# Kernel tuning notes

Measured on AMD Instinct MI355X. Metric: run time of the kernel, lower is better.

Reference implementation:

```python
import jax, jax.numpy as jnp
import numpy as np

WORD_VOCAB = 100000
TAG_VOCAB = 50
WD = 300
TD = 100
EMB = WD + TD          # 400: LSTM input size AND hidden size
H = EMB
L = 512


def setup_inputs() -> dict:
    key = jax.random.key(0)
    ks = jax.random.split(key, 16)
    def p(k, shape):
        return jax.random.normal(k, shape, dtype=jnp.float32) * 0.05
    return {
        "words_idx_tensor": jax.random.randint(ks[0], (1, L), 0, WORD_VOCAB),
        "tags_idx_tensor": jax.random.randint(ks[1], (1, L), 0, TAG_VOCAB),
        "max_length": L,
        "word_emb": p(ks[2], (WORD_VOCAB, WD)),
        "tag_emb": p(ks[3], (TAG_VOCAB, TD)),
        # stacked [fwd, bwd] directions per layer (PyTorch LSTM gate order i,f,g,o)
        "w_ih_l0": p(ks[4], (2, 4 * H, EMB)),
        "w_hh_l0": p(ks[5], (2, 4 * H, H)),
        "b_ih_l0": p(ks[6], (2, 4 * H)),
        "b_hh_l0": p(ks[7], (2, 4 * H)),
        "w_ih_l1": p(ks[8], (2, 4 * H, 2 * H)),
        "w_hh_l1": p(ks[9], (2, 4 * H, H)),
        "b_ih_l1": p(ks[10], (2, 4 * H)),
        "b_hh_l1": p(ks[11], (2, 4 * H)),
        "fc1_w": p(ks[12], (1, 4 * H)),
        "fc1_b": p(ks[13], (1,)),
    }


def _lstm_dir(x, w_ih, w_hh, b_ih, b_hh, reverse):
    # x: [T, in]. Precompute input projections once (hoisted out of scan).
    xi = x @ w_ih.T + b_ih + b_hh  # [T, 4H]
    Hn = w_hh.shape[1]

    def step(carry, g_in):
        h, c = carry
        g = g_in + h @ w_hh.T
        i, f, gg, o = jnp.split(g, 4, axis=-1)
        c = jax.nn.sigmoid(f) * c + jax.nn.sigmoid(i) * jnp.tanh(gg)
        h = jax.nn.sigmoid(o) * jnp.tanh(c)
        return (h, c), h

    init = (jnp.zeros((Hn,), x.dtype), jnp.zeros((Hn,), x.dtype))
    _, hs = jax.lax.scan(step, init, xi, reverse=reverse)
    return hs  # [T, H]


def _bilstm(x, w_ih, w_hh, b_ih, b_hh):
    fwd = _lstm_dir(x, w_ih[0], w_hh[0], b_ih[0], b_hh[0], False)
    bwd = _lstm_dir(x, w_ih[1], w_hh[1], b_ih[1], b_hh[1], True)
    return jnp.concatenate([fwd, bwd], axis=-1)  # [T, 2H]


def reference(words_idx_tensor, tags_idx_tensor, max_length, word_emb, tag_emb,
              w_ih_l0, w_hh_l0, b_ih_l0, b_hh_l0,
              w_ih_l1, w_hh_l1, b_ih_l1, b_hh_l1,
              fc1_w, fc1_b):
    # Embedding lookup + concat; batch dim of size 1 squeezed (torch's
    # view(shape[1], shape[0], -1) yields [L, 1, emb] for the LSTM).
    x = jnp.concatenate([word_emb[words_idx_tensor[0]],
                         tag_emb[tags_idx_tensor[0]]], axis=-1)  # [L, EMB]

    h = _bilstm(x, w_ih_l0, w_hh_l0, b_ih_l0, b_hh_l0)   # [L, 2H]
    h = _bilstm(h, w_ih_l1, w_hh_l1, b_ih_l1, b_hh_l1)   # [L, 2H]

    # Pairwise edge scores: tanh(W @ [h_i; h_j] + b).
    # Split W into head/dep halves -> two small GEMMs + broadcast outer-sum,
    # avoiding the O(L^2 * 4H) concatenated feature tensor.
    two_h = fc1_w.shape[1] // 2
    s = h @ fc1_w[:, :two_h].T   # [L, 1]
    t = h @ fc1_w[:, two_h:].T   # [L, 1]
    scores = jnp.tanh(s[:, None, :] + t[None, :, :] + fc1_b)  # [L, L, 1]
    # torch stacks (i outer, j inner) -> [L*L, 1, 1]
    return scores.reshape(max_length * max_length, 1, 1)
```

## Files before the change

kernel.cpp:

```cpp
#include <hip/hip_runtime.h>

#define SEQ 512
#define HID 400
#define GATES 1600
#define E1 800
#define TEAM 25
#define RECGRID 256
#define ROWS 64
#define HSL 16

__device__ __forceinline__ float bf2f(unsigned short u) {
    return __uint_as_float(((unsigned)u) << 16);
}
__device__ __forceinline__ unsigned short f2bf(float f) {
    unsigned u = __float_as_uint(f);
    u += 0x7FFFu + ((u >> 16) & 1u);
    return (unsigned short)(u >> 16);
}
__device__ __forceinline__ float sigm(float x) { return 1.f / (1.f + __expf(-x)); }
__device__ __forceinline__ float tanh_f(float x) {
    float xc = fminf(fmaxf(x, -15.f), 15.f);
    float e = __expf(2.f * xc);
    return (e - 1.f) / (e + 1.f);
}
__device__ __forceinline__ float loadx(const void* p, size_t i, int isbf) {
    return isbf ? bf2f(((const unsigned short*)p)[i]) : ((const float*)p)[i];
}

__global__ void detect_kernel(const unsigned short* __restrict__ wemb,
                              unsigned* __restrict__ dtf) {
    __shared__ int cnt;
    if (threadIdx.x == 0) cnt = 0;
    __syncthreads();
    int pass = 0;
    for (int i = 0; i < 8; ++i) {
        unsigned short u = wemb[threadIdx.x * 8 + i];
        int e = (u >> 7) & 0xFF;
        pass += (e >= 100 && e <= 130) ? 1 : 0;
    }
    atomicAdd(&cnt, pass);
    __syncthreads();
    if (threadIdx.x == 0) *dtf = (cnt >= 1843) ? 1u : 0u;
}

__global__ void embed_kernel(const int* __restrict__ words, const int* __restrict__ tags,
                             const void* __restrict__ wemb, const void* __restrict__ temb,
                             float* __restrict__ x ,
                             const unsigned* __restrict__ dtf) {
    int t = blockIdx.x;
    int w = words[t], g = tags[t];
    int isbf = (int)*dtf;
    for (int k = threadIdx.x; k < HID; k += blockDim.x) {
        float v = (k < 300) ? loadx(wemb, (size_t)w * 300 + k, isbf)
                            : loadx(temb, (size_t)g * 100 + (k - 300), isbf);
        x[(size_t)t * HID + k] = v;
    }
}

__global__ __launch_bounds__(256) void proj_kernel(
        const void* __restrict__ Araw, int tagged,
        const void* __restrict__ Wraw ,
        const void* __restrict__ bihRaw, const void* __restrict__ bhhRaw,
        float* __restrict__ xi ,
        int K, const unsigned* __restrict__ dtf) {
    const int isbf = (int)*dtf;
    __shared__ float As[16][132];
    __shared__ float Ws[16][68];
    int tid = threadIdx.x;
    int t0 = blockIdx.x * 128, n0 = blockIdx.y * 64, dir = blockIdx.z;
    int arow = tid >> 1, akoff = (tid & 1) * 8;
    int wrow = tid >> 2, wkoff = (tid & 3) * 4;
    int tx = (tid & 15) * 4;
    int ty = (tid >> 4) * 8;

    const float* Af = (const float*)Araw + (size_t)(t0 + arow) * K + akoff;
    const unsigned long long* At = (const unsigned long long*)Araw +
                                   (size_t)(t0 + arow) * K + akoff;
    size_t wbase = (size_t)(dir * GATES + n0 + wrow) * K + wkoff;
    const float* Wf = (const float*)Wraw + wbase;
    const unsigned short* Wh = (const unsigned short*)Wraw + wbase;

    float acc[8][4] = {};
    for (int k0 = 0; k0 < K; k0 += 16) {
        float av8[8];
        if (tagged) {
            ulonglong2 q0 = *(const ulonglong2*)(At + k0);
            ulonglong2 q1 = *(const ulonglong2*)(At + k0 + 2);
            ulonglong2 q2 = *(const ulonglong2*)(At + k0 + 4);
            ulonglong2 q3 = *(const ulonglong2*)(At + k0 + 6);
            av8[0] = __uint_as_float((unsigned)q0.x); av8[1] = __uint_as_float((unsigned)q0.y);
            av8[2] = __uint_as_float((unsigned)q1.x); av8[3] = __uint_as_float((unsigned)q1.y);
            av8[4] = __uint_as_float((unsigned)q2.x); av8[5] = __uint_as_float((unsigned)q2.y);
            av8[6] = __uint_as_float((unsigned)q3.x); av8[7] = __uint_as_float((unsigned)q3.y);
        } else {
            float4 a0 = *(const float4*)(Af + k0);
            float4 a1 = *(const float4*)(Af + k0 + 4);
            av8[0] = a0.x; av8[1] = a0.y; av8[2] = a0.z; av8[3] = a0.w;
            av8[4] = a1.x; av8[5] = a1.y; av8[6] = a1.z; av8[7] = a1.w;
        }
        float4 wv;
        if (isbf) {
            ushort4 w4 = *(const ushort4*)(Wh + k0);
            wv = make_float4(bf2f(w4.x), bf2f(w4.y), bf2f(w4.z), bf2f(w4.w));
        } else {
            wv = *(const float4*)(Wf + k0);
        }
        __syncthreads();
#pragma unroll
        for (int i = 0; i < 8; ++i) As[akoff + i][arow] = av8[i];
        Ws[wkoff + 0][wrow] = wv.x; Ws[wkoff + 1][wrow] = wv.y;
        Ws[wkoff + 2][wrow] = wv.z; Ws[wkoff + 3][wrow] = wv.w;
        __syncthreads();
#pragma unroll
        for (int kk = 0; kk < 16; ++kk) {
            float4 alo = *(const float4*)&As[kk][ty];
            float4 ahi = *(const float4*)&As[kk][ty + 4];
            float4 w4  = *(const float4*)&Ws[kk][tx];
            float av[8] = {alo.x, alo.y, alo.z, alo.w, ahi.x, ahi.y, ahi.z, ahi.w};
            float wvv[4] = {w4.x, w4.y, w4.z, w4.w};
#pragma unroll
            for (int i = 0; i < 8; ++i)
#pragma unroll
                for (int j = 0; j < 4; ++j)
                    acc[i][j] = fmaf(av[i], wvv[j], acc[i][j]);
        }
    }
    float bias[4];
#pragma unroll
    for (int j = 0; j < 4; ++j) {
        int n = n0 + tx + j;
        bias[j] = loadx(bihRaw, dir * GATES + n, isbf) + loadx(bhhRaw, dir * GATES + n, isbf);
    }
    float* xout = xi + (size_t)dir * SEQ * GATES;
#pragma unroll
    for (int i = 0; i < 8; ++i) {
        int t = t0 + ty + i;
        float4 o = make_float4(acc[i][0] + bias[0], acc[i][1] + bias[1],
                               acc[i][2] + bias[2], acc[i][3] + bias[3]);
        *(float4*)&xout[(size_t)t * GATES + n0 + tx] = o;
    }
}

struct SyncArea { unsigned cnt[8]; unsigned claim[2]; unsigned pad[6]; };

__global__ __launch_bounds__(512, 2) void rec_kernel(
        const float* __restrict__ xi ,
        const void* __restrict__ whhRaw ,
        unsigned long long* __restrict__ hx  ,
        unsigned long long* __restrict__ hx2 ,
        unsigned tagbase, SyncArea* __restrict__ sy,
        const unsigned* __restrict__ dtf) {
    int tid = threadIdx.x;
    __shared__ int role[2];
    if (tid == 0) {
        unsigned xcd = __builtin_amdgcn_s_getreg((3 << 11) | 20) & 0xFu;
        unsigned rank = atomicAdd(&sy->cnt[xcd], 1u);
        unsigned group = rank / TEAM;
        unsigned key = 1u + xcd * 64u + group;
        if ((rank % TEAM) == TEAM - 1) {
            unsigned prev = atomicCAS(&sy->claim[0], 0u, key);
            if (prev != 0u) atomicCAS(&sy->claim[1], 0u, key);
        }
        int dir = -1;
        while (dir < 0) {
            unsigned c0 = __hip_atomic_load(&sy->claim[0], __ATOMIC_RELAXED,
                                            __HIP_MEMORY_SCOPE_AGENT);
            unsigned c1 = __hip_atomic_load(&sy->claim[1], __ATOMIC_RELAXED,
                                            __HIP_MEMORY_SCOPE_AGENT);
            if (c0 == key) dir = 0;
            else if (c1 == key) dir = 1;
            else if (c0 != 0u && c1 != 0u) dir = 2;
        }
        role[0] = dir;
        role[1] = (int)(rank % TEAM);
    }
    __syncthreads();
    const int dir = role[0];
    const int wg  = role[1];
    if (dir == 2) return;

    const int chunk = tid & 15;
    const int rg    = tid >> 4;
    const int isbf  = (int)*dtf;
    const int dirHID = dir * HID;

    __shared__ __align__(16) float hbuf[16 * 28];
    __shared__ __align__(16) float partials[ROWS][20];
    __shared__ __align__(16) float gates[ROWS];

    float wv[2][25];
#pragma unroll
    for (int r = 0; r < 2; ++r) {
        int lr = rg * 2 + r;
        int jj = lr >> 2, gg = lr & 3;
        int grow = gg * HID + wg * HSL + jj;
        size_t base = ((size_t)dir * GATES + grow) * HID + chunk * 25;
        if (isbf) {
            const unsigned short* p = (const unsigned short*)whhRaw + base;
#pragma unroll
            for (int c = 0; c < 25; ++c) wv[r][c] = bf2f(p[c]);
        } else {
            const float* p = (const float*)whhRaw + base;
#pragma unroll
            for (int c = 0; c < 25; ++c) wv[r][c] = p[c];
        }
    }

    int xrow = 0;
    if (tid < ROWS) { int jj = tid >> 2, gg = tid & 3; xrow = gg * HID + wg * HSL + jj; }
    const int hIdx = (tid / 25) * 28 + (tid % 25);
    const float* xibase = xi + (size_t)dir * SEQ * GATES;
    float cstate = 0.f;
    size_t myelem = dirHID + wg * HSL + tid;

#pragma unroll 1
    for (int k = 0; k < SEQ; ++k) {
        int t = dir ? (SEQ - 1 - k) : k;
        float xiv = 0.f;
        if (tid < ROWS) xiv = xibase[(size_t)t * GATES + xrow];

        if (k > 0) {
            int tprev = dir ? (t + 1) : (t - 1);
            if (tid < HID) {
                const unsigned want = tagbase + (unsigned)k;
                size_t eidx = (size_t)tprev * E1 + dirHID + tid;
                const volatile unsigned long long* p =
                    (const volatile unsigned long long*)&hx[eidx];
                unsigned long long w;
                int spin = 0;
                for (;;) {
                    w = *p;
                    if ((unsigned)(w >> 32) == want) break;
                    if (++spin >= 24) {
                        w = __hip_atomic_load(&hx2[eidx], __ATOMIC_RELAXED,
                                              __HIP_MEMORY_SCOPE_AGENT);
                        if ((unsigned)(w >> 32) == want) break;
                        spin = 0;
                    }
                }
                hbuf[hIdx] = __uint_as_float((unsigned)w);
            }
        } else {
            if (tid < HID) hbuf[hIdx] = 0.f;
        }
        __syncthreads();

        const float* hb = &hbuf[chunk * 28];
        float4 h4a = *(const float4*)(hb + 0);
        float4 h4b = *(const float4*)(hb + 4);
        float4 h4c = *(const float4*)(hb + 8);
        float4 h4d = *(const float4*)(hb + 12);
        float4 h4e = *(const float4*)(hb + 16);
        float4 h4f = *(const float4*)(hb + 20);
        float hv[25] = {h4a.x, h4a.y, h4a.z, h4a.w, h4b.x, h4b.y, h4b.z, h4b.w,
                        h4c.x, h4c.y, h4c.z, h4c.w, h4d.x, h4d.y, h4d.z, h4d.w,
                        h4e.x, h4e.y, h4e.z, h4e.w, h4f.x, h4f.y, h4f.z, h4f.w,
                        hb[24]};
        float acc0 = 0.f, acc1 = 0.f;
#pragma unroll
        for (int c = 0; c < 25; ++c) {
            acc0 = fmaf(wv[0][c], hv[c], acc0);
            acc1 = fmaf(wv[1][c], hv[c], acc1);
        }
        partials[rg * 2 + 0][chunk] = acc0;
        partials[rg * 2 + 1][chunk] = acc1;
        __syncthreads();

        if (tid < ROWS) {
            const float4* pr = (const float4*)&partials[tid][0];
            float4 p0 = pr[0], p1 = pr[1], p2 = pr[2], p3 = pr[3];
            float s = p0.x + p0.y + p0.z + p0.w
                    + p1.x + p1.y + p1.z + p1.w
                    + p2.x + p2.y + p2.z + p2.w
                    + p3.x + p3.y + p3.z + p3.w;
            gates[tid] = s + xiv;
        }
        __syncthreads();

        if (tid < HSL) {
            float4 g4 = *(const float4*)&gates[tid * 4];
            float ig = sigm(g4.x), fg = sigm(g4.y), cg = tanh_f(g4.z), og = sigm(g4.w);
            cstate = fg * cstate + ig * cg;
            float hv2 = og * tanh_f(cstate);
            unsigned long long w =
                ((unsigned long long)(tagbase + (unsigned)k + 1u) << 32) |
                (unsigned long long)(unsigned)__float_as_uint(hv2);
            size_t eidx = (size_t)t * E1 + myelem;
            *(volatile unsigned long long*)&hx[eidx] = w;
            __hip_atomic_store(&hx2[eidx], w, __ATOMIC_RELAXED,
                               __HIP_MEMORY_SCOPE_AGENT);
        }
    }
}

__global__ void st_kernel(const unsigned long long* __restrict__ h1x ,
                          const void* __restrict__ fw ,
                          float* __restrict__ sv, float* __restrict__ tv,
                          const unsigned* __restrict__ dtf) {
    int i = blockIdx.x;
    int lane = threadIdx.x;
    int isbf = (int)*dtf;
    float s = 0.f, t = 0.f;
    for (int j = lane; j < E1; j += 64) {
        float hv = __uint_as_float((unsigned)h1x[(size_t)i * E1 + j]);
        s += hv * loadx(fw, j, isbf);
        t += hv * loadx(fw, E1 + j, isbf);
    }
#pragma unroll
    for (int o = 32; o > 0; o >>= 1) {
        s += __shfl_xor(s, o, 64);
        t += __shfl_xor(t, o, 64);
    }
    if (lane == 0) { sv[i] = s; tv[i] = t; }
}

__global__ void scores_kernel(const float* __restrict__ sv, const float* __restrict__ tv,
                              const void* __restrict__ fb, void* __restrict__ out,
                              const unsigned* __restrict__ dtf) {
    int idx = blockIdx.x * blockDim.x + threadIdx.x;
    int i = idx >> 9, j = idx & 511;
    int isbf = (int)*dtf;
    float v = tanh_f(sv[i] + tv[j] + loadx(fb, 0, isbf));
    if (isbf) ((unsigned short*)out)[idx] = f2bf(v);
    else      ((float*)out)[idx] = v;
}

static constexpr size_t OFF_X    = 0;
static constexpr size_t OFF_XI   = 819200;
static constexpr size_t OFF_SV   = 7372800;
static constexpr size_t OFF_TV   = 7374848;
static constexpr size_t OFF_DTF  = 7376896;
static constexpr size_t OFF_SYNC = 7376960;
static constexpr size_t OFF_HX   = 7377216;
static constexpr size_t OFF_HX2  = 10654016;

extern "C" void kernel_launch(void* const* d_in, const int* in_sizes, int n_in,
                              void* d_out, int out_size, void* d_ws, size_t ws_size,
                              hipStream_t stream) {
    const int* words = (const int*)d_in[0];
    const int* tags  = (const int*)d_in[1];
    const void* wemb = d_in[3];
    const void* temb = d_in[4];
    const void* wih0 = d_in[5];
    const void* whh0 = d_in[6];
    const void* bih0 = d_in[7];
    const void* bhh0 = d_in[8];
    const void* wih1 = d_in[9];
    const void* whh1 = d_in[10];
    const void* bih1 = d_in[11];
    const void* bhh1 = d_in[12];
    const void* fw   = d_in[13];
    const void* fb   = d_in[14];

    char* ws = (char*)d_ws;
    float* x               = (float*)(ws + OFF_X);
    float* xi              = (float*)(ws + OFF_XI);
    float* sv              = (float*)(ws + OFF_SV);
    float* tv              = (float*)(ws + OFF_TV);
    unsigned* dtf          = (unsigned*)(ws + OFF_DTF);
    SyncArea* sync0        = (SyncArea*)(ws + OFF_SYNC);
    SyncArea* sync1        = (SyncArea*)(ws + OFF_SYNC + 64);
    unsigned long long* hx  = (unsigned long long*)(ws + OFF_HX);
    unsigned long long* hx2 = (unsigned long long*)(ws + OFF_HX2);

    hipMemsetAsync(ws + OFF_SYNC, 0, 128, stream);
    detect_kernel<<<1, 256, 0, stream>>>((const unsigned short*)wemb, dtf);
    embed_kernel<<<SEQ, 128, 0, stream>>>(words, tags, wemb, temb, x, dtf);

    proj_kernel<<<dim3(4, 25, 2), 256, 0, stream>>>(x, 0, wih0, bih0, bhh0, xi, HID, dtf);
    rec_kernel<<<RECGRID, 512, 0, stream>>>(xi, whh0, hx, hx2, 0u, sync0, dtf);

    proj_kernel<<<dim3(4, 25, 2), 256, 0, stream>>>(hx, 1, wih1, bih1, bhh1, xi, E1, dtf);
    rec_kernel<<<RECGRID, 512, 0, stream>>>(xi, whh1, hx, hx2, 512u, sync1, dtf);

    st_kernel<<<SEQ, 64, 0, stream>>>(hx, fw, sv, tv, dtf);
    scores_kernel<<<(SEQ * SEQ) / 256, 256, 0, stream>>>(sv, tv, fb, d_out, dtf);
}
```

Before: 1.791 ms.

## Use sc0 inline-asm polling, prefetch next input gates, move publishing to idle wave

Replaces the volatile loads and stores used for inter-block h exchange with inline-asm global loads and stores carrying the sc0 cache bit, and raises the spin count before falling back to the atomic copy. Prefetches the next timestep's input-projection value after the barrier so its latency overlaps the matvec, instead of loading it at the top of each step. Moves the gate nonlinearity and publish work from threads 0-15 to threads 448-463, a wave that does not take part in polling. Intent is to cut per-step latency on the serial recurrence critical path. Risk: the inline asm waits on all outstanding loads, and the cache-coherence behaviour of sc0 across CUs must hold.

```diff
diff --git a/kernel.cpp b/kernel.cpp
--- a/kernel.cpp
+++ b/kernel.cpp
@@ -25,6 +25,18 @@
 }
 __device__ __forceinline__ float loadx(const void* p, size_t i, int isbf) {
     return isbf ? bf2f(((const unsigned short*)p)[i]) : ((const float*)p)[i];
+}
+
+__device__ __forceinline__ unsigned long long load_sc0(const unsigned long long* p) {
+    unsigned long long v;
+    asm volatile("global_load_dwordx2 %0, %1, off sc0\n\t"
+                 "s_waitcnt vmcnt(0)"
+                 : "=&v"(v) : "v"(p) : "memory");
+    return v;
+}
+__device__ __forceinline__ void store_sc0(unsigned long long* p, unsigned long long v) {
+    asm volatile("global_store_dwordx2 %0, %1, off sc0"
+                 :: "v"(p), "v"(v) : "memory");
 }
 
 __global__ void detect_kernel(const unsigned short* __restrict__ wemb,
@@ -210,28 +222,31 @@
     if (tid < ROWS) { int jj = tid >> 2, gg = tid & 3; xrow = gg * HID + wg * HSL + jj; }
     const int hIdx = (tid / 25) * 28 + (tid % 25);
     const float* xibase = xi + (size_t)dir * SEQ * GATES;
+    const int pub = tid - 448;
     float cstate = 0.f;
-    size_t myelem = dirHID + wg * HSL + tid;
+    size_t myelem = dirHID + wg * HSL + (pub & 15);
+
+    float xiv = 0.f;
+    {
+        int tf = dir ? (SEQ - 1) : 0;
+        if (tid < ROWS) xiv = xibase[(size_t)tf * GATES + xrow];
+    }
 
 #pragma unroll 1
     for (int k = 0; k < SEQ; ++k) {
         int t = dir ? (SEQ - 1 - k) : k;
-        float xiv = 0.f;
-        if (tid < ROWS) xiv = xibase[(size_t)t * GATES + xrow];
 
         if (k > 0) {
             int tprev = dir ? (t + 1) : (t - 1);
             if (tid < HID) {
                 const unsigned want = tagbase + (unsigned)k;
                 size_t eidx = (size_t)tprev * E1 + dirHID + tid;
-                const volatile unsigned long long* p =
-                    (const volatile unsigned long long*)&hx[eidx];
                 unsigned long long w;
                 int spin = 0;
                 for (;;) {
-                    w = *p;
+                    w = load_sc0(&hx[eidx]);
                     if ((unsigned)(w >> 32) == want) break;
-                    if (++spin >= 24) {
+                    if (++spin >= 32) {
                         w = __hip_atomic_load(&hx2[eidx], __ATOMIC_RELAXED,
                                               __HIP_MEMORY_SCOPE_AGENT);
                         if ((unsigned)(w >> 32) == want) break;
@@ -244,6 +259,12 @@
             if (tid < HID) hbuf[hIdx] = 0.f;
         }
         __syncthreads();
+
+        float xiv_next = 0.f;
+        if (k + 1 < SEQ && tid < ROWS) {
+            int tn = dir ? (t - 1) : (t + 1);
+            xiv_next = xibase[(size_t)tn * GATES + xrow];
+        }
 
         const float* hb = &hbuf[chunk * 28];
         float4 h4a = *(const float4*)(hb + 0);
@@ -277,8 +298,8 @@
         }
         __syncthreads();
 
-        if (tid < HSL) {
-            float4 g4 = *(const float4*)&gates[tid * 4];
+        if (pub >= 0 && pub < HSL) {
+            float4 g4 = *(const float4*)&gates[pub * 4];
             float ig = sigm(g4.x), fg = sigm(g4.y), cg = tanh_f(g4.z), og = sigm(g4.w);
             cstate = fg * cstate + ig * cg;
             float hv2 = og * tanh_f(cstate);
@@ -286,10 +307,11 @@
                 ((unsigned long long)(tagbase + (unsigned)k + 1u) << 32) |
                 (unsigned long long)(unsigned)__float_as_uint(hv2);
             size_t eidx = (size_t)t * E1 + myelem;
-            *(volatile unsigned long long*)&hx[eidx] = w;
+            store_sc0(&hx[eidx], w);
             __hip_atomic_store(&hx2[eidx], w, __ATOMIC_RELAXED,
                                __HIP_MEMORY_SCOPE_AGENT);
         }
+        xiv = xiv_next;
     }
 }
 
```

Result: slower. 4.834 ms (+169.9%).
